# Kernel tuning notes

Hardware: AMD Instinct MI355X
Metric: run time of the kernel (lower is better)

The kernel has to match this reference:

```python
import jax, jax.numpy as jnp
import numpy as np

V = 50000  # item vocab (input_size == output_size)
H = 256    # hidden_size
B = 512    # batch_size


def setup_inputs() -> dict:
    key = jax.random.key(0)
    ks = jax.random.split(key, 8)
    return {
        "input_ids": jax.random.randint(ks[0], (B,), 0, V),
        "hidden": jax.random.normal(ks[1], (1, B, H), jnp.float32),
        # GRU layer-0 params, PyTorch layout: gates stacked as [r, z, n]
        "w_ih": jax.random.normal(ks[2], (3 * H, V), jnp.float32) * 0.02,
        "w_hh": jax.random.normal(ks[3], (3 * H, H), jnp.float32) * 0.05,
        "b_ih": jax.random.normal(ks[4], (3 * H,), jnp.float32) * 0.01,
        "b_hh": jax.random.normal(ks[5], (3 * H,), jnp.float32) * 0.01,
        # h2o linear
        "w_out": jax.random.normal(ks[6], (V, H), jnp.float32) * 0.02,
        "b_out": jax.random.normal(ks[7], (V,), jnp.float32) * 0.01,
    }


def _gru_step(one_hot, h0, w_ih, w_hh, b_ih, b_hh):
    # one-hot scatter feeding the input-to-hidden GEMM (as in the torch module)
    gi = one_hot @ w_ih.T + b_ih          # [B, 3H]
    gh = h0 @ w_hh.T + b_hh               # [B, 3H]
    i_r, i_z, i_n = jnp.split(gi, 3, axis=-1)
    h_r, h_z, h_n = jnp.split(gh, 3, axis=-1)
    r = jax.nn.sigmoid(i_r + h_r)
    z = jax.nn.sigmoid(i_z + h_z)
    n = jnp.tanh(i_n + r * h_n)
    return (1.0 - z) * n + z * h0         # [B, H]


def reference(input_ids, hidden, w_ih, w_hh, b_ih, b_hh, w_out, b_out):
    # onehot_encode: zero buffer + scatter 1.0 at item index
    one_hot = jnp.zeros((B, V), w_ih.dtype).at[jnp.arange(B), input_ids].set(1.0)
    h1 = _gru_step(one_hot, hidden[0], w_ih, w_hh, b_ih, b_hh)  # [B, H]
    logit = jnp.tanh(h1 @ w_out.T + b_out)                      # final_activation = Tanh
    return logit, h1[None]  # ([B, V], [1, B, H])
```

## Files before the change

### kernel.cpp

```cpp
#include <hip/hip_runtime.h>
#include <hip/hip_bf16.h>

#define V 50000
#define H 256
#define B 512

typedef __bf16 bf16x8 __attribute__((ext_vector_type(8)));
typedef float f32x4 __attribute__((ext_vector_type(4)));

__device__ __forceinline__ float tanh_fast(float x) {
    float a = __builtin_fabsf(x);
    float e = __expf(2.0f * a);
    float r = fmaf(-2.0f, __builtin_amdgcn_rcpf(e + 1.0f), 1.0f);
    return __builtin_copysignf(r, x);
}

__global__ __launch_bounds__(256) void gru_h1_kernel(
    const int* __restrict__ ids, const float* __restrict__ h0,
    const float* __restrict__ w_ih, const float* __restrict__ w_hh,
    const float* __restrict__ b_ih, const float* __restrict__ b_hh,
    float* __restrict__ h1_out, __bf16* __restrict__ h1b)
{
    __shared__ float h0s[2 * 256];
    const int t = threadIdx.x;
    const int b0 = blockIdx.x * 2;

#pragma unroll
    for (int i = 0; i < 2; i++)
        h0s[i * 256 + t] = h0[(b0 + i) * 256 + t];
    __syncthreads();

    const int j = t;

    int id[2];
    float gir[2], giz[2], gin[2];
#pragma unroll
    for (int m = 0; m < 2; m++) {
        id[m] = ids[b0 + m];
        gir[m] = w_ih[(size_t)j * V + id[m]];
        giz[m] = w_ih[(size_t)(H + j) * V + id[m]];
        gin[m] = w_ih[(size_t)(2 * H + j) * V + id[m]];
    }

    float ar[2] = {0.f, 0.f}, az[2] = {0.f, 0.f}, an[2] = {0.f, 0.f};
    const float* __restrict__ wr_p = w_hh + (size_t)j * H;
    const float* __restrict__ wz_p = w_hh + (size_t)(H + j) * H;
    const float* __restrict__ wn_p = w_hh + (size_t)(2 * H + j) * H;

#pragma unroll 4
    for (int k = 0; k < H; k += 4) {
        f32x4 wr = *(const f32x4*)(wr_p + k);
        f32x4 wz = *(const f32x4*)(wz_p + k);
        f32x4 wn = *(const f32x4*)(wn_p + k);
#pragma unroll
        for (int m = 0; m < 2; m++) {
            f32x4 h = *(const f32x4*)&h0s[m * 256 + k];
#pragma unroll
            for (int u = 0; u < 4; u++) {
                ar[m] = fmaf(wr[u], h[u], ar[m]);
                az[m] = fmaf(wz[u], h[u], az[m]);
                an[m] = fmaf(wn[u], h[u], an[m]);
            }
        }
    }

    const float bir = b_ih[j], biz = b_ih[H + j], bin = b_ih[2 * H + j];
    const float bhr = b_hh[j], bhz = b_hh[H + j], bhn = b_hh[2 * H + j];

#pragma unroll
    for (int m = 0; m < 2; m++) {
        float r = 1.f / (1.f + __expf(-(gir[m] + bir + ar[m] + bhr)));
        float z = 1.f / (1.f + __expf(-(giz[m] + biz + az[m] + bhz)));
        float n = tanh_fast(gin[m] + bin + an[m] + bhn * r + r * an[m] * 0.f
                            + r * (an[m] * 0.f));
        n = tanh_fast(gin[m] + bin + r * (an[m] + bhn));
        float h1 = (1.f - z) * n + z * h0s[m * 256 + j];
        h1_out[(b0 + m) * H + j] = h1;
        h1b[(b0 + m) * H + j] = (__bf16)h1;
    }
}

#define BN 64
#define BSTR 264

__global__ __launch_bounds__(256, 4) void logit_kernel(
    const __bf16* __restrict__ h1b, const float* __restrict__ w_out,
    const float* __restrict__ b_out, float* __restrict__ out)
{
    __shared__ __bf16 Bs[BN * BSTR];
    const int t = threadIdx.x;
    const int n0 = blockIdx.x * BN;
    const int m_tile = blockIdx.y;

    {
        const int c4 = t & 63;
        const int v0 = t >> 6;
#pragma unroll
        for (int half = 0; half < 2; half++) {
            f32x4 g[8];
#pragma unroll
            for (int i = 0; i < 8; i++) {
                int n = n0 + v0 + (half * 8 + i) * 4;
                g[i] = (f32x4){0.f, 0.f, 0.f, 0.f};
                if (n < V) g[i] = *(const f32x4*)(w_out + (size_t)n * H + c4 * 4);
            }
#pragma unroll
            for (int i = 0; i < 8; i++) {
                int v = v0 + (half * 8 + i) * 4;
                struct alignas(8) BH4 { __bf16 h[4]; } p;
                p.h[0] = (__bf16)g[i][0];
                p.h[1] = (__bf16)g[i][1];
                p.h[2] = (__bf16)g[i][2];
                p.h[3] = (__bf16)g[i][3];
                *(BH4*)&Bs[v * BSTR + c4 * 4] = p;
            }
        }
    }
    __syncthreads();

    const int lane = t & 63;
    const int wave = t >> 6;
    const int q = lane >> 4;
    const int v16 = lane & 15;
    const int m_base = m_tile * 256 + wave * 64;

    f32x4 acc[4][4];
#pragma unroll
    for (int i = 0; i < 4; i++)
#pragma unroll
        for (int jj = 0; jj < 4; jj++) acc[i][jj] = (f32x4){0.f, 0.f, 0.f, 0.f};

    const __bf16* a_base = h1b + (m_base + v16) * H + q * 8;

#pragma unroll
    for (int ks = 0; ks < 8; ks++) {
        bf16x8 a[4];
#pragma unroll
        for (int i = 0; i < 4; i++)
            a[i] = *(const bf16x8*)(a_base + i * 16 * H + ks * 32);
#pragma unroll
        for (int jj = 0; jj < 4; jj++) {
            bf16x8 bfr = *(const bf16x8*)&Bs[(jj * 16 + v16) * BSTR + ks * 32 + q * 8];
#pragma unroll
            for (int i = 0; i < 4; i++)
                acc[i][jj] = __builtin_amdgcn_mfma_f32_16x16x32_bf16(
                    bfr, a[i], acc[i][jj], 0, 0, 0);
        }
    }

#pragma unroll
    for (int jj = 0; jj < 4; jj++) {
        const int n = n0 + jj * 16 + q * 4;
        if (n < V) {
            f32x4 bo = *(const f32x4*)&b_out[n];
#pragma unroll
            for (int i = 0; i < 4; i++) {
                f32x4 r;
#pragma unroll
                for (int u = 0; u < 4; u++)
                    r[u] = tanh_fast(acc[i][jj][u] + bo[u]);
                *(f32x4*)&out[(size_t)(m_base + i * 16 + v16) * V + n] = r;
            }
        }
    }
}

extern "C" void kernel_launch(void* const* d_in, const int* in_sizes, int n_in,
                              void* d_out, int out_size, void* d_ws, size_t ws_size,
                              hipStream_t stream) {
    const int* ids = (const int*)d_in[0];
    const float* hidden = (const float*)d_in[1];
    const float* w_ih = (const float*)d_in[2];
    const float* w_hh = (const float*)d_in[3];
    const float* b_ih = (const float*)d_in[4];
    const float* b_hh = (const float*)d_in[5];
    const float* w_out = (const float*)d_in[6];
    const float* b_out = (const float*)d_in[7];

    float* out = (float*)d_out;
    float* h1_out = out + (size_t)B * V;
    __bf16* h1b = (__bf16*)d_ws;

    gru_h1_kernel<<<256, 256, 0, stream>>>(ids, hidden, w_ih, w_hh, b_ih, b_hh,
                                           h1_out, h1b);

    dim3 grid((V + BN - 1) / BN, 2);
    logit_kernel<<<grid, 256, 0, stream>>>(h1b, w_out, b_out, out);
}
```

Before: 333.4 us.

## Cover all batch rows per logit block and split GRU reduction across two halves

The logit kernel now uses 512-thread blocks that each cover all 512 batch rows, so every w_out tile is loaded and converted to bf16 only once instead of twice (grid y dimension removed). The GRU kernel doubles its threads and splits the K reduction of the recurrent matvec between two halves, combining the partial sums through shared memory. It also uses a reciprocal intrinsic for the sigmoid. The larger blocks may lower occupancy, and the logit grid now has half as many blocks.

Result: slower. 346.5 us (+3.9%).

```diff
diff --git a/kernel.cpp b/kernel.cpp
--- a/kernel.cpp
+++ b/kernel.cpp
@@ -15,105 +15,116 @@
     return __builtin_copysignf(r, x);
 }
 
-__global__ __launch_bounds__(256) void gru_h1_kernel(
+__device__ __forceinline__ float sigmoid_fast(float x) {
+    return __builtin_amdgcn_rcpf(1.0f + __expf(-x));
+}
+
+__global__ __launch_bounds__(512) void gru_h1_kernel(
     const int* __restrict__ ids, const float* __restrict__ h0,
     const float* __restrict__ w_ih, const float* __restrict__ w_hh,
     const float* __restrict__ b_ih, const float* __restrict__ b_hh,
     float* __restrict__ h1_out, __bf16* __restrict__ h1b)
 {
-    __shared__ float h0s[2 * 256];
+    __shared__ float h0s[2][H];
+    __shared__ float part[2][3][H];
     const int t = threadIdx.x;
+    const int j = t & (H - 1);
+    const int half = t >> 8;
     const int b0 = blockIdx.x * 2;
 
+    const int id0 = ids[b0], id1 = ids[b0 + 1];
+    float gi[2][3];
+    if (half == 0) {
 #pragma unroll
-    for (int i = 0; i < 2; i++)
-        h0s[i * 256 + t] = h0[(b0 + i) * 256 + t];
+        for (int g = 0; g < 3; g++) {
+            gi[0][g] = w_ih[(size_t)(g * H + j) * V + id0];
+            gi[1][g] = w_ih[(size_t)(g * H + j) * V + id1];
+        }
+    }
+    h0s[half][j] = h0[(b0 + half) * H + j];
     __syncthreads();
 
-    const int j = t;
-
-    int id[2];
-    float gir[2], giz[2], gin[2];
-#pragma unroll
-    for (int m = 0; m < 2; m++) {
-        id[m] = ids[b0 + m];
-        gir[m] = w_ih[(size_t)j * V + id[m]];
-        giz[m] = w_ih[(size_t)(H + j) * V + id[m]];
-        gin[m] = w_ih[(size_t)(2 * H + j) * V + id[m]];
-    }
+    const int k0 = half * (H / 2);
+    const float* __restrict__ wr = w_hh + (size_t)(0 * H + j) * H + k0;
+    const float* __restrict__ wz = w_hh + (size_t)(1 * H + j) * H + k0;
+    const float* __restrict__ wn = w_hh + (size_t)(2 * H + j) * H + k0;
 
     float ar[2] = {0.f, 0.f}, az[2] = {0.f, 0.f}, an[2] = {0.f, 0.f};
-    const float* __restrict__ wr_p = w_hh + (size_t)j * H;
-    const float* __restrict__ wz_p = w_hh + (size_t)(H + j) * H;
-    const float* __restrict__ wn_p = w_hh + (size_t)(2 * H + j) * H;
-
 #pragma unroll 4
-    for (int k = 0; k < H; k += 4) {
-        f32x4 wr = *(const f32x4*)(wr_p + k);
-        f32x4 wz = *(const f32x4*)(wz_p + k);
-        f32x4 wn = *(const f32x4*)(wn_p + k);
+    for (int k = 0; k < H / 2; k += 4) {
+        f32x4 vr = *(const f32x4*)(wr + k);
+        f32x4 vz = *(const f32x4*)(wz + k);
+        f32x4 vn = *(const f32x4*)(wn + k);
 #pragma unroll
         for (int m = 0; m < 2; m++) {
-            f32x4 h = *(const f32x4*)&h0s[m * 256 + k];
+            f32x4 h = *(const f32x4*)&h0s[m][k0 + k];
 #pragma unroll
             for (int u = 0; u < 4; u++) {
-                ar[m] = fmaf(wr[u], h[u], ar[m]);
-                az[m] = fmaf(wz[u], h[u], az[m]);
-                an[m] = fmaf(wn[u], h[u], an[m]);
+                ar[m] = fmaf(vr[u], h[u], ar[m]);
+                az[m] = fmaf(vz[u], h[u], az[m]);
+                an[m] = fmaf(vn[u], h[u], an[m]);
             }
         }
     }
 
-    const float bir = b_ih[j], biz = b_ih[H + j], bin = b_ih[2 * H + j];
-    const float bhr = b_hh[j], bhz = b_hh[H + j], bhn = b_hh[2 * H + j];
+    if (half == 1) {
+#pragma unroll
+        for (int m = 0; m < 2; m++) {
+            part[m][0][j] = ar[m];
+            part[m][1][j] = az[m];
+            part[m][2][j] = an[m];
+        }
+    }
+    __syncthreads();
 
+    if (half == 0) {
+        const float bir = b_ih[j], biz = b_ih[H + j], bin = b_ih[2 * H + j];
+        const float bhr = b_hh[j], bhz = b_hh[H + j], bhn = b_hh[2 * H + j];
 #pragma unroll
-    for (int m = 0; m < 2; m++) {
-        float r = 1.f / (1.f + __expf(-(gir[m] + bir + ar[m] + bhr)));
-        float z = 1.f / (1.f + __expf(-(giz[m] + biz + az[m] + bhz)));
-        float n = tanh_fast(gin[m] + bin + an[m] + bhn * r + r * an[m] * 0.f
-                            + r * (an[m] * 0.f));
-        n = tanh_fast(gin[m] + bin + r * (an[m] + bhn));
-        float h1 = (1.f - z) * n + z * h0s[m * 256 + j];
-        h1_out[(b0 + m) * H + j] = h1;
-        h1b[(b0 + m) * H + j] = (__bf16)h1;
+        for (int m = 0; m < 2; m++) {
+            float sr = ar[m] + part[m][0][j];
+            float sz = az[m] + part[m][1][j];
+            float sn = an[m] + part[m][2][j];
+            float r = sigmoid_fast(gi[m][0] + bir + sr + bhr);
+            float z = sigmoid_fast(gi[m][1] + biz + sz + bhz);
+            float n = tanh_fast(gi[m][2] + bin + r * (sn + bhn));
+            float h1 = (1.f - z) * n + z * h0s[m][j];
+            h1_out[(b0 + m) * H + j] = h1;
+            h1b[(b0 + m) * H + j] = (__bf16)h1;
+        }
     }
 }
 
 #define BN 64
 #define BSTR 264
 
-__global__ __launch_bounds__(256, 4) void logit_kernel(
+__global__ __launch_bounds__(512) void logit_kernel(
     const __bf16* __restrict__ h1b, const float* __restrict__ w_out,
     const float* __restrict__ b_out, float* __restrict__ out)
 {
     __shared__ __bf16 Bs[BN * BSTR];
     const int t = threadIdx.x;
     const int n0 = blockIdx.x * BN;
-    const int m_tile = blockIdx.y;
 
     {
         const int c4 = t & 63;
         const int v0 = t >> 6;
+        f32x4 g[8];
 #pragma unroll
-        for (int half = 0; half < 2; half++) {
-            f32x4 g[8];
+        for (int i = 0; i < 8; i++) {
+            const int n = n0 + v0 * 8 + i;
+            g[i] = (f32x4){0.f, 0.f, 0.f, 0.f};
+            if (n < V) g[i] = *(const f32x4*)(w_out + (size_t)n * H + c4 * 4);
+        }
 #pragma unroll
-            for (int i = 0; i < 8; i++) {
-                int n = n0 + v0 + (half * 8 + i) * 4;
-                g[i] = (f32x4){0.f, 0.f, 0.f, 0.f};
-                if (n < V) g[i] = *(const f32x4*)(w_out + (size_t)n * H + c4 * 4);
-            }
-#pragma unroll
-            for (int i = 0; i < 8; i++) {
-                int v = v0 + (half * 8 + i) * 4;
-                struct alignas(8) BH4 { __bf16 h[4]; } p;
-                p.h[0] = (__bf16)g[i][0];
-                p.h[1] = (__bf16)g[i][1];
-                p.h[2] = (__bf16)g[i][2];
-                p.h[3] = (__bf16)g[i][3];
-                *(BH4*)&Bs[v * BSTR + c4 * 4] = p;
-            }
+        for (int i = 0; i < 8; i++) {
+            const int v = v0 * 8 + i;
+            struct alignas(8) BH4 { __bf16 h[4]; } p;
+            p.h[0] = (__bf16)g[i][0];
+            p.h[1] = (__bf16)g[i][1];
+            p.h[2] = (__bf16)g[i][2];
+            p.h[3] = (__bf16)g[i][3];
+            *(BH4*)&Bs[v * BSTR + c4 * 4] = p;
         }
     }
     __syncthreads();
@@ -122,7 +133,7 @@
     const int wave = t >> 6;
     const int q = lane >> 4;
     const int v16 = lane & 15;
-    const int m_base = m_tile * 256 + wave * 64;
+    const int m_base = wave * 64;
 
     f32x4 acc[4][4];
 #pragma unroll
@@ -130,7 +141,7 @@
 #pragma unroll
         for (int jj = 0; jj < 4; jj++) acc[i][jj] = (f32x4){0.f, 0.f, 0.f, 0.f};
 
-    const __bf16* a_base = h1b + (m_base + v16) * H + q * 8;
+    const __bf16* a_base = h1b + (size_t)(m_base + v16) * H + q * 8;
 
 #pragma unroll
     for (int ks = 0; ks < 8; ks++) {
@@ -181,9 +192,8 @@
     float* h1_out = out + (size_t)B * V;
     __bf16* h1b = (__bf16*)d_ws;
 
-    gru_h1_kernel<<<256, 256, 0, stream>>>(ids, hidden, w_ih, w_hh, b_ih, b_hh,
+    gru_h1_kernel<<<256, 512, 0, stream>>>(ids, hidden, w_ih, w_hh, b_ih, b_hh,
                                            h1_out, h1b);
 
-    dim3 grid((V + BN - 1) / BN, 2);
-    logit_kernel<<<grid, 256, 0, stream>>>(h1b, w_out, b_out, out);
+    logit_kernel<<<(V + BN - 1) / BN, 512, 0, stream>>>(h1b, w_out, b_out, out);
 }
```
